# Performance work log

Hardware: AMD Instinct MI355X
Metric: run time of the kernel (lower is better)

Reference implementation:

```python
import jax, jax.numpy as jnp
import numpy as np

EMBED = 128
HEADS = 32
HEAD_DIM = EMBED // HEADS  # 4
BATCH = 32
SEQ = 2048


def setup_inputs() -> dict:
    key = jax.random.key(0)
    ks = jax.random.split(key, 6)
    s = 1.0 / np.sqrt(EMBED)
    return {
        "x": jax.random.normal(ks[0], (BATCH, SEQ, EMBED), dtype=jnp.float32),
        # torch Linear weights are (out_features, in_features)
        "Wq": jax.random.uniform(ks[1], (EMBED, EMBED), jnp.float32, -s, s),
        "Wk": jax.random.uniform(ks[2], (EMBED, EMBED), jnp.float32, -s, s),
        "Wv": jax.random.uniform(ks[3], (EMBED, EMBED), jnp.float32, -s, s),
        "Wo": jax.random.uniform(ks[4], (EMBED, EMBED), jnp.float32, -s, s),
        "bo": jax.random.uniform(ks[5], (EMBED,), jnp.float32, -s, s),
    }


def reference(x, Wq, Wk, Wv, Wo, bo):
    b, s, e = x.shape
    h, d = HEADS, HEAD_DIM
    # projections (torch Linear: x @ W.T)
    q = (x @ Wq.T).reshape(b, s, h, d)
    k = (x @ Wk.T).reshape(b, s, h, d)
    v = (x @ Wv.T).reshape(b, s, h, d)
    # FAITHFUL to source: einsum 'bnqh,bnkh->bnqk' on (b, seq, heads, head_dim)
    # => n = seq position, q/k = HEADS. Attention is over the heads axis.
    scale = 1.0 / (float(d) ** 0.5)
    scores = jnp.einsum('bnqh,bnkh->bnqk', q, k) * scale  # (b, seq, heads, heads)
    attn = jax.nn.softmax(scores, axis=-1)
    attended = jnp.einsum('bnqk,bnkv->bnqv', attn, v).reshape(b, s, e)
    return attended @ Wo.T + bo
```

## Files before the change

kernel.cpp:

```cpp
#include <hip/hip_runtime.h>


#define TOKENS (32 * 2048)
#define E 128
#define NH 32
#define BT 16
#define THREADS 128
#define LPITCH 136

typedef __attribute__((ext_vector_type(8))) short short8;
typedef __attribute__((ext_vector_type(4))) float f32x4;
typedef __fp16 h2_t __attribute__((ext_vector_type(2)));
typedef __fp16 h8_t __attribute__((ext_vector_type(8)));

#if __has_builtin(__builtin_amdgcn_exp2f)
#define EXP2F __builtin_amdgcn_exp2f
#else
#define EXP2F exp2f
#endif

#if __has_builtin(__builtin_amdgcn_rcpf)
#define RCPF __builtin_amdgcn_rcpf
#else
#define RCPF(x) (1.0f / (x))
#endif

static __device__ __forceinline__ unsigned short f2bf(float f) {
    unsigned u = __float_as_uint(f);
    unsigned r = (u + 0x7fffu + ((u >> 16) & 1u)) >> 16;
    return (unsigned short)r;
}

static __device__ __forceinline__ unsigned pk16(float a, float b) {
    return __builtin_bit_cast(unsigned, __builtin_amdgcn_cvt_pkrtz(a, b));
}
static __device__ __forceinline__ h2_t u2h(unsigned u) {
    return __builtin_bit_cast(h2_t, u);
}

static __device__ __forceinline__ float fdot2(h2_t a, h2_t b, float c) {
#if __has_builtin(__builtin_amdgcn_fdot2)
    return __builtin_amdgcn_fdot2(a, b, c, false);
#else
    return (float)a.x * (float)b.x + (float)a.y * (float)b.y + c;
#endif
}

__global__ void pack_w(const float* __restrict__ Wq, const float* __restrict__ Wk,
                       const float* __restrict__ Wv, const float* __restrict__ Wo,
                       unsigned short* __restrict__ wpk) {
    int idx = blockIdx.x * blockDim.x + threadIdx.x;
    if (idx >= 4 * 8 * 4 * 64) return;
    int lane = idx & 63;
    int ks   = (idx >> 6) & 3;
    int nt   = (idx >> 8) & 7;
    int proj = idx >> 11;
    const float* W = (proj == 0) ? Wq : (proj == 1) ? Wk : (proj == 2) ? Wv : Wo;
    int c = lane & 15, g = lane >> 4;
    const float* src = W + (size_t)(nt * 16 + c) * E + ks * 32 + g * 8;
    unsigned short* dst = wpk + (size_t)idx * 8;
    if (proj < 3) {
#pragma unroll
        for (int j = 0; j < 8; ++j) dst[j] = f2bf(src[j]);
    } else {
#pragma unroll
        for (int j = 0; j < 8; ++j)
            dst[j] = __builtin_bit_cast(unsigned short, (__fp16)src[j]);
    }
}

__global__ __launch_bounds__(THREADS) void mha_fused(
        const float* __restrict__ x, const unsigned short* __restrict__ wpk,
        const float* __restrict__ bo, float* __restrict__ out) {
    __shared__ __fp16 qs [BT * LPITCH];
    __shared__ __fp16 ksh[BT * LPITCH];
    __shared__ __fp16 vth[BT * LPITCH];
    __shared__ __fp16 at_[BT * LPITCH];

    const int tid  = threadIdx.x;
    const int wave = tid >> 6;
    const int lane = tid & 63;
    const int c = lane & 15, g = lane >> 4;
    const int bt0 = blockIdx.x * BT;

    {
        short8 afrag[4];
        const float* xrow = x + (size_t)(bt0 + c) * E;
#pragma unroll
        for (int ks2 = 0; ks2 < 4; ++ks2) {
            const float* p = xrow + ks2 * 32 + g * 8;
            float4 v0 = *(const float4*)(p);
            float4 v1 = *(const float4*)(p + 4);
            short8 a;
            a[0] = f2bf(v0.x); a[1] = f2bf(v0.y); a[2] = f2bf(v0.z); a[3] = f2bf(v0.w);
            a[4] = f2bf(v1.x); a[5] = f2bf(v1.y); a[6] = f2bf(v1.z); a[7] = f2bf(v1.w);
            afrag[ks2] = a;
        }

#pragma unroll
        for (int i = 0; i < 12; ++i) {
            int nc   = wave * 12 + i;
            int proj = nc >> 3;
            int nt   = nc & 7;
            const unsigned short* wb = wpk + ((size_t)((proj * 8 + nt) * 4) * 64 + lane) * 8;
            f32x4 acc = {0.f, 0.f, 0.f, 0.f};
#pragma unroll
            for (int ks2 = 0; ks2 < 4; ++ks2) {
                short8 b = *(const short8*)(wb + (size_t)ks2 * 64 * 8);
                acc = __builtin_amdgcn_mfma_f32_16x16x32_bf16(afrag[ks2], b, acc, 0, 0, 0);
            }
            int col = nt * 16 + c;
            if (proj < 2) {
                __fp16* dst = proj ? ksh : qs;
#pragma unroll
                for (int r2 = 0; r2 < 4; ++r2) {
                    int row = g * 4 + r2;
                    dst[row * LPITCH + col] = (__fp16)acc[r2];
                }
            } else {
                int vc = (col & 3) * 32 + (col >> 2);
#pragma unroll
                for (int r2 = 0; r2 < 4; ++r2) {
                    int row = g * 4 + r2;
                    vth[row * LPITCH + vc] = (__fp16)acc[r2];
                }
            }
        }
    }
    __syncthreads();

    {
        const float cexp = 0.5f * 1.44269504088896340736f;
        const int tok = tid >> 3;
        const int qb  = tid & 7;
        const __fp16* krow = ksh + tok * LPITCH;
        const __fp16* vrow = vth + tok * LPITCH;
        const __fp16* qrow = qs  + tok * LPITCH;
#pragma unroll 1
        for (int hlf = 0; hlf < 2; ++hlf) {
            const int qhA = qb + hlf * 8;
            const int qhB = qhA + 16;
            uint2 qrA = *(const uint2*)(qrow + qhA * 4);
            uint2 qrB = *(const uint2*)(qrow + qhB * 4);
            h2_t qA0 = u2h(qrA.x), qA1 = u2h(qrA.y);
            h2_t qB0 = u2h(qrB.x), qB1 = u2h(qrB.y);
            float sumA = 0.f, sumB = 0.f;
            unsigned pkA[16], pkB[16];
#pragma unroll
            for (int kp = 0; kp < 16; ++kp) {
                uint4 kr = *(const uint4*)(krow + kp * 8);
                float sA0 = fdot2(u2h(kr.x), qA0, fdot2(u2h(kr.y), qA1, 0.f));
                float sA1 = fdot2(u2h(kr.z), qA0, fdot2(u2h(kr.w), qA1, 0.f));
                float sB0 = fdot2(u2h(kr.x), qB0, fdot2(u2h(kr.y), qB1, 0.f));
                float sB1 = fdot2(u2h(kr.z), qB0, fdot2(u2h(kr.w), qB1, 0.f));
                float eA0 = EXP2F(sA0 * cexp), eA1 = EXP2F(sA1 * cexp);
                float eB0 = EXP2F(sB0 * cexp), eB1 = EXP2F(sB1 * cexp);
                sumA += eA0 + eA1; sumB += eB0 + eB1;
                pkA[kp] = pk16(eA0, eA1);
                pkB[kp] = pk16(eB0, eB1);
            }
            float aA[4], aB[4];
#pragma unroll
            for (int d = 0; d < 4; ++d) {
                float accA = 0.f, accB = 0.f;
#pragma unroll
                for (int vp = 0; vp < 4; ++vp) {
                    uint4 vr = *(const uint4*)(vrow + d * 32 + vp * 8);
                    accA = fdot2(u2h(pkA[vp * 4 + 0]), u2h(vr.x), accA);
                    accA = fdot2(u2h(pkA[vp * 4 + 1]), u2h(vr.y), accA);
                    accA = fdot2(u2h(pkA[vp * 4 + 2]), u2h(vr.z), accA);
                    accA = fdot2(u2h(pkA[vp * 4 + 3]), u2h(vr.w), accA);
                    accB = fdot2(u2h(pkB[vp * 4 + 0]), u2h(vr.x), accB);
                    accB = fdot2(u2h(pkB[vp * 4 + 1]), u2h(vr.y), accB);
                    accB = fdot2(u2h(pkB[vp * 4 + 2]), u2h(vr.z), accB);
                    accB = fdot2(u2h(pkB[vp * 4 + 3]), u2h(vr.w), accB);
                }
                aA[d] = accA; aB[d] = accB;
            }
            float rA = RCPF(sumA), rB = RCPF(sumB);
            __fp16* atr = at_ + tok * LPITCH;
            uint2 stA, stB;
            stA.x = pk16(aA[0] * rA, aA[1] * rA);
            stA.y = pk16(aA[2] * rA, aA[3] * rA);
            stB.x = pk16(aB[0] * rB, aB[1] * rB);
            stB.y = pk16(aB[2] * rB, aB[3] * rB);
            *(uint2*)(atr + qhA * 4) = stA;
            *(uint2*)(atr + qhB * 4) = stB;
        }
    }
    __syncthreads();

    {
        h8_t af[4];
#pragma unroll
        for (int ks2 = 0; ks2 < 4; ++ks2) {
            af[ks2] = *(const h8_t*)(at_ + c * LPITCH + ks2 * 32 + g * 8);
        }
#pragma unroll
        for (int i = 0; i < 4; ++i) {
            int nt = wave * 4 + i;
            const unsigned short* wb = wpk + ((size_t)((3 * 8 + nt) * 4) * 64 + lane) * 8;
            f32x4 acc = {0.f, 0.f, 0.f, 0.f};
#pragma unroll
            for (int ks2 = 0; ks2 < 4; ++ks2) {
                h8_t b = *(const h8_t*)(wb + (size_t)ks2 * 64 * 8);
                acc = __builtin_amdgcn_mfma_f32_16x16x32_f16(af[ks2], b, acc, 0, 0, 0);
            }
            int col = nt * 16 + c;
            float bias = bo[col];
            float* orow = out + (size_t)(bt0 + g * 4) * E + col;
#pragma unroll
            for (int r2 = 0; r2 < 4; ++r2) {
                orow[(size_t)r2 * E] = acc[r2] + bias;
            }
        }
    }
}

extern "C" void kernel_launch(void* const* d_in, const int* in_sizes, int n_in,
                              void* d_out, int out_size, void* d_ws, size_t ws_size,
                              hipStream_t stream) {
    const float* x  = (const float*)d_in[0];
    const float* Wq = (const float*)d_in[1];
    const float* Wk = (const float*)d_in[2];
    const float* Wv = (const float*)d_in[3];
    const float* Wo = (const float*)d_in[4];
    const float* bo = (const float*)d_in[5];
    unsigned short* wpk = (unsigned short*)d_ws;
    float* out = (float*)d_out;

    pack_w<<<32, 256, 0, stream>>>(Wq, Wk, Wv, Wo, wpk);
    mha_fused<<<TOKENS / BT, THREADS, 0, stream>>>(x, wpk, bo, out);
}
```

Measured before the change: 50.74 us.

## Compute per-token head-attention scores and PV with 32x32 MFMA instead of fdot2

Replaces the scalar fdot2-based per-token 32x32 head attention with matrix-core work: one 32x32x16 f16 MFMA for QK^T per token (K padded with zeros) and two MFMAs for P·V. V is stored in a permuted layout so the MFMA output registers line up, and a row of ones is injected to produce the softmax denominator inside the MFMA. The aim is to offload the dot-product ALU work to matrix cores. In exchange, half the K dimension is zero padding, exp is computed on accumulator registers, and a shuffle and extra LDS layout logic are needed.

```diff
diff --git a/kernel.cpp b/kernel.cpp
--- a/kernel.cpp
+++ b/kernel.cpp
@@ -10,6 +10,7 @@
 
 typedef __attribute__((ext_vector_type(8))) short short8;
 typedef __attribute__((ext_vector_type(4))) float f32x4;
+typedef __attribute__((ext_vector_type(16))) float f32x16;
 typedef __fp16 h2_t __attribute__((ext_vector_type(2)));
 typedef __fp16 h8_t __attribute__((ext_vector_type(8)));
 
@@ -34,16 +35,16 @@
 static __device__ __forceinline__ unsigned pk16(float a, float b) {
     return __builtin_bit_cast(unsigned, __builtin_amdgcn_cvt_pkrtz(a, b));
 }
-static __device__ __forceinline__ h2_t u2h(unsigned u) {
-    return __builtin_bit_cast(h2_t, u);
-}
-
-static __device__ __forceinline__ float fdot2(h2_t a, h2_t b, float c) {
-#if __has_builtin(__builtin_amdgcn_fdot2)
-    return __builtin_amdgcn_fdot2(a, b, c, false);
-#else
-    return (float)a.x * (float)b.x + (float)a.y * (float)b.y + c;
-#endif
+
+static __device__ __forceinline__ f32x16 zero16() {
+    f32x16 z;
+#pragma unroll
+    for (int i = 0; i < 16; ++i) z[i] = 0.f;
+    return z;
+}
+
+static __device__ __forceinline__ int vperm(int kh) {
+    return ((kh >> 4) & 1) * 16 + ((kh >> 2) & 1) * 8 + ((kh >> 3) & 1) * 4 + (kh & 3);
 }
 
 __global__ void pack_w(const float* __restrict__ Wq, const float* __restrict__ Wk,
@@ -118,7 +119,7 @@
                     dst[row * LPITCH + col] = (__fp16)acc[r2];
                 }
             } else {
-                int vc = (col & 3) * 32 + (col >> 2);
+                int vc = (col & 3) * 32 + vperm(col >> 2);
 #pragma unroll
                 for (int r2 = 0; r2 < 4; ++r2) {
                     int row = g * 4 + r2;
@@ -131,61 +132,61 @@
 
     {
         const float cexp = 0.5f * 1.44269504088896340736f;
-        const int tok = tid >> 3;
-        const int qb  = tid & 7;
-        const __fp16* krow = ksh + tok * LPITCH;
-        const __fp16* vrow = vth + tok * LPITCH;
-        const __fp16* qrow = qs  + tok * LPITCH;
-#pragma unroll 1
-        for (int hlf = 0; hlf < 2; ++hlf) {
-            const int qhA = qb + hlf * 8;
-            const int qhB = qhA + 16;
-            uint2 qrA = *(const uint2*)(qrow + qhA * 4);
-            uint2 qrB = *(const uint2*)(qrow + qhB * 4);
-            h2_t qA0 = u2h(qrA.x), qA1 = u2h(qrA.y);
-            h2_t qB0 = u2h(qrB.x), qB1 = u2h(qrB.y);
-            float sumA = 0.f, sumB = 0.f;
-            unsigned pkA[16], pkB[16];
-#pragma unroll
-            for (int kp = 0; kp < 16; ++kp) {
-                uint4 kr = *(const uint4*)(krow + kp * 8);
-                float sA0 = fdot2(u2h(kr.x), qA0, fdot2(u2h(kr.y), qA1, 0.f));
-                float sA1 = fdot2(u2h(kr.z), qA0, fdot2(u2h(kr.w), qA1, 0.f));
-                float sB0 = fdot2(u2h(kr.x), qB0, fdot2(u2h(kr.y), qB1, 0.f));
-                float sB1 = fdot2(u2h(kr.z), qB0, fdot2(u2h(kr.w), qB1, 0.f));
-                float eA0 = EXP2F(sA0 * cexp), eA1 = EXP2F(sA1 * cexp);
-                float eB0 = EXP2F(sB0 * cexp), eB1 = EXP2F(sB1 * cexp);
-                sumA += eA0 + eA1; sumB += eB0 + eB1;
-                pkA[kp] = pk16(eA0, eA1);
-                pkB[kp] = pk16(eB0, eB1);
-            }
-            float aA[4], aB[4];
-#pragma unroll
-            for (int d = 0; d < 4; ++d) {
-                float accA = 0.f, accB = 0.f;
-#pragma unroll
-                for (int vp = 0; vp < 4; ++vp) {
-                    uint4 vr = *(const uint4*)(vrow + d * 32 + vp * 8);
-                    accA = fdot2(u2h(pkA[vp * 4 + 0]), u2h(vr.x), accA);
-                    accA = fdot2(u2h(pkA[vp * 4 + 1]), u2h(vr.y), accA);
-                    accA = fdot2(u2h(pkA[vp * 4 + 2]), u2h(vr.z), accA);
-                    accA = fdot2(u2h(pkA[vp * 4 + 3]), u2h(vr.w), accA);
-                    accB = fdot2(u2h(pkB[vp * 4 + 0]), u2h(vr.x), accB);
-                    accB = fdot2(u2h(pkB[vp * 4 + 1]), u2h(vr.y), accB);
-                    accB = fdot2(u2h(pkB[vp * 4 + 2]), u2h(vr.z), accB);
-                    accB = fdot2(u2h(pkB[vp * 4 + 3]), u2h(vr.w), accB);
-                }
-                aA[d] = accA; aB[d] = accB;
-            }
-            float rA = RCPF(sumA), rB = RCPF(sumB);
-            __fp16* atr = at_ + tok * LPITCH;
-            uint2 stA, stB;
-            stA.x = pk16(aA[0] * rA, aA[1] * rA);
-            stA.y = pk16(aA[2] * rA, aA[3] * rA);
-            stB.x = pk16(aB[0] * rB, aB[1] * rB);
-            stB.y = pk16(aB[2] * rB, aB[3] * rB);
-            *(uint2*)(atr + qhA * 4) = stA;
-            *(uint2*)(atr + qhB * 4) = stB;
+        const int c32 = lane & 31;
+        const int gg  = lane >> 5;
+        const uint4 ONES4 = make_uint4(0x3C003C00u, 0x3C003C00u, 0x3C003C00u, 0x3C003C00u);
+#pragma unroll 2
+        for (int t8 = 0; t8 < 8; ++t8) {
+            const int tok = wave * 8 + t8;
+            const __fp16* qrow = qs  + tok * LPITCH;
+            const __fp16* krow = ksh + tok * LPITCH;
+            const __fp16* vrow = vth + tok * LPITCH;
+
+            uint4 kraw = {0u, 0u, 0u, 0u}, qraw = {0u, 0u, 0u, 0u};
+            if (gg == 0) {
+                uint2 kk = *(const uint2*)(krow + c32 * 4);
+                uint2 qq = *(const uint2*)(qrow + c32 * 4);
+                kraw.x = kk.x; kraw.y = kk.y;
+                qraw.x = qq.x; qraw.y = qq.y;
+            }
+            h8_t kf = __builtin_bit_cast(h8_t, kraw);
+            h8_t qf = __builtin_bit_cast(h8_t, qraw);
+
+            f32x16 sc = zero16();
+            sc = __builtin_amdgcn_mfma_f32_32x32x16_f16(kf, qf, sc, 0, 0, 0);
+
+            float e[16];
+#pragma unroll
+            for (int r = 0; r < 16; ++r) e[r] = EXP2F(sc[r] * cexp);
+            uint4 p0u = make_uint4(pk16(e[0], e[1]),  pk16(e[2], e[3]),
+                                   pk16(e[4], e[5]),  pk16(e[6], e[7]));
+            uint4 p1u = make_uint4(pk16(e[8], e[9]),  pk16(e[10], e[11]),
+                                   pk16(e[12], e[13]), pk16(e[14], e[15]));
+            h8_t p0 = __builtin_bit_cast(h8_t, p0u);
+            h8_t p1 = __builtin_bit_cast(h8_t, p1u);
+
+            uint4 vr0 = *(const uint4*)(vrow + (c32 & 3) * 32 + gg * 8);
+            uint4 vr1 = *(const uint4*)(vrow + (c32 & 3) * 32 + 16 + gg * 8);
+            if (c32 == 4) { vr0 = ONES4; vr1 = ONES4; }
+            h8_t v0f = __builtin_bit_cast(h8_t, vr0);
+            h8_t v1f = __builtin_bit_cast(h8_t, vr1);
+
+            f32x16 pv = zero16();
+            pv = __builtin_amdgcn_mfma_f32_32x32x16_f16(v0f, p0, pv, 0, 0, 0);
+            pv = __builtin_amdgcn_mfma_f32_32x32x16_f16(v1f, p1, pv, 0, 0, 0);
+
+            float sum  = __shfl(pv[0], c32 + 32, 64);
+            float rinv = RCPF(sum);
+            if (lane < 32) {
+                unsigned short h0 = __builtin_bit_cast(unsigned short, (__fp16)(pv[0] * rinv));
+                unsigned short h1 = __builtin_bit_cast(unsigned short, (__fp16)(pv[1] * rinv));
+                unsigned short h2 = __builtin_bit_cast(unsigned short, (__fp16)(pv[2] * rinv));
+                unsigned short h3 = __builtin_bit_cast(unsigned short, (__fp16)(pv[3] * rinv));
+                uint2 st;
+                st.x = (unsigned)h0 | ((unsigned)h1 << 16);
+                st.y = (unsigned)h2 | ((unsigned)h3 << 16);
+                *(uint2*)(at_ + tok * LPITCH + c32 * 4) = st;
+            }
         }
     }
     __syncthreads();
```

Result: faster. 46.08 us (-9.2%).
